# Kernel tuning notes

Measured on AMD Instinct MI355X. Metric: run time of the kernel, lower is better.

Reference implementation:

```python
import jax, jax.numpy as jnp
import numpy as np

E, M, K, I, TOPK = 8, 4096, 2048, 1408, 2
N = 2 * I  # gated: w1 produces [gate, up]


def setup_inputs() -> dict:
    key = jax.random.key(0)
    k1, k2, k3, k4, k5 = jax.random.split(key, 5)
    hidden_states = jax.random.normal(k1, (M, K), dtype=jnp.float32)
    w1 = jax.random.normal(k2, (E, N, K), dtype=jnp.float32) * 0.02
    w2 = jax.random.normal(k3, (E, K, I), dtype=jnp.float32) * 0.02
    raw = jax.random.uniform(k4, (M, TOPK), dtype=jnp.float32)
    topk_weights = raw / jnp.sum(raw, axis=-1, keepdims=True)  # router probs
    topk_ids = jax.random.randint(k5, (M, TOPK), 0, E, dtype=jnp.int32)
    return {
        "hidden_states": hidden_states,
        "w1": w1,
        "w2": w2,
        "topk_weights": topk_weights,
        "topk_ids": topk_ids,
    }


def reference(hidden_states, w1, w2, topk_weights, topk_ids):
    # MoE: permute -> grouped GEMM1 -> silu_and_mul -> grouped GEMM2 -> unpermute+reduce.
    # Dense-per-expert formulation (math-equivalent to grouped GEMM over routed tokens).
    # GEMM1: [E, M, N]
    h1 = jnp.einsum("mk,enk->emn", hidden_states, w1)
    gate, up = h1[..., :I], h1[..., I:]
    act = jax.nn.silu(gate) * up  # silu_and_mul, [E, M, I]
    # GEMM2: [E, M, K]
    y = jnp.einsum("emi,eki->emk", act, w2)
    # Unpermute: gather each token's topk expert outputs, apply router weights, reduce.
    y_tok = jnp.transpose(y, (1, 0, 2))  # [M, E, K]
    sel = jnp.take_along_axis(y_tok, topk_ids[:, :, None].astype(jnp.int32), axis=1)  # [M, topk, K]
    out = jnp.sum(sel * topk_weights[:, :, None], axis=1)  # [M, K]
    return out
```

## Files before the change

kernel.cpp:

```cpp
#include <hip/hip_runtime.h>
#include <hip/hip_bf16.h>
#include <stdint.h>

#define EXPERTS 8
#define MTOK 4096
#define KDIM 2048
#define IDIM 1408
#define NDIM 2816
#define CAP  8192

typedef __attribute__((ext_vector_type(8))) short bf16x8;
typedef __attribute__((ext_vector_type(4))) float f32x4;

__device__ __forceinline__ unsigned short f2bf(float x) {
    unsigned u = __float_as_uint(x);
    u = u + 0x7fffu + ((u >> 16) & 1u);
    return (unsigned short)(u >> 16);
}

__device__ __forceinline__ void gload16(const void* g, void* l) {
    __builtin_amdgcn_global_load_lds(
        (const __attribute__((address_space(1))) void*)g,
        (__attribute__((address_space(3))) void*)l, 16, 0, 0);
}

__global__ void __launch_bounds__(256) conv_bf16(const float* __restrict__ src,
                                                 unsigned short* __restrict__ dst, int n4) {
    int i = blockIdx.x * 256 + threadIdx.x;
    int st = gridDim.x * 256;
    for (; i < n4; i += st) {
        float4 v = reinterpret_cast<const float4*>(src)[i];
        ushort4 r;
        r.x = f2bf(v.x); r.y = f2bf(v.y); r.z = f2bf(v.z); r.w = f2bf(v.w);
        reinterpret_cast<ushort4*>(dst)[i] = r;
    }
}

__global__ void __launch_bounds__(256) router(const float* __restrict__ tw,
                                              const int* __restrict__ ids,
                                              int* __restrict__ tok, float* __restrict__ wgt,
                                              int* __restrict__ cnt) {
    int m = blockIdx.x * 256 + threadIdx.x;
    if (m >= MTOK) return;
#pragma unroll
    for (int t = 0; t < 2; t++) {
        int e = ids[m * 2 + t];
        int slot = atomicAdd(&cnt[e], 1);
        tok[e * CAP + slot] = m;
        wgt[e * CAP + slot] = tw[m * 2 + t];
    }
}

__global__ void scan_off(const int* __restrict__ cnt, int* __restrict__ off) {
    if (threadIdx.x == 0) {
        int s = 0;
        for (int e = 0; e < EXPERTS; e++) { off[e] = s; s += cnt[e]; }
    }
}

__global__ void __launch_bounds__(512, 2) gemm1_silu(
    const unsigned short* __restrict__ hsb,
    const unsigned short* __restrict__ w1b,
    const int* __restrict__ tok,
    const int* __restrict__ cnt,
    const int* __restrict__ off,
    unsigned short* __restrict__ act) {
    const int cb = blockIdx.x;
    const int rb = blockIdx.y;
    const int e  = blockIdx.z;
    const int cnt_e = cnt[e];
    if (rb * 128 >= cnt_e) return;
    const int off_e = off[e];
    const int NT = KDIM / 64;

    __shared__ __align__(16) char smem[147456];
    __shared__ int toks[128];

    const int tid = threadIdx.x;
    const int lane = tid & 63;
    const int w = tid >> 6;
    if (tid < 128) {
        int slot = rb * 128 + tid;
        toks[tid] = (slot < cnt_e) ? tok[e * CAP + slot] : 0;
    }
    __syncthreads();

    size_t sA[2]; int dA[2];
#pragma unroll
    for (int c = 0; c < 2; c++) {
        int i = c * 512 + tid;
        int row = i >> 3, gp = i & 7, gl = gp ^ (row & 7);
        sA[c] = (size_t)toks[row] * KDIM + gl * 8;
        dA[c] = i * 16;
    }
    size_t sB[4]; int dB[4];
    const size_t w1base = (size_t)e * (size_t)NDIM * KDIM;
#pragma unroll
    for (int c = 0; c < 4; c++) {
        int j = c * 512 + tid;
        int row = j >> 3, gp = j & 7, gl = gp ^ (row & 7);
        int G = row >> 4;
        int w1row = ((G & 1) ? IDIM : 0) + cb * 128 + (G >> 1) * 16 + (row & 15);
        sB[c] = w1base + (size_t)w1row * KDIM + gl * 8;
        dB[c] = 16384 + j * 16;
    }

    const int wr = w >> 2, wc = w & 3;
    const int l16 = lane & 15, lg = lane >> 4;
    int aoff[4][2], boff[4][2];
#pragma unroll
    for (int m = 0; m < 4; m++) {
        int row = wr * 64 + m * 16 + l16;
#pragma unroll
        for (int h = 0; h < 2; h++)
            aoff[m][h] = row * 128 + (((h * 4 + lg) ^ (row & 7)) * 16);
    }
#pragma unroll
    for (int n = 0; n < 4; n++) {
        int row = wc * 64 + n * 16 + l16;
#pragma unroll
        for (int h = 0; h < 2; h++)
            boff[n][h] = 16384 + row * 128 + (((h * 4 + lg) ^ (row & 7)) * 16);
    }

    f32x4 acc[4][4];
#pragma unroll
    for (int m = 0; m < 4; m++)
#pragma unroll
        for (int n = 0; n < 4; n++) acc[m][n] = {0.f, 0.f, 0.f, 0.f};

#define STG_A(t, base) { const int ko_ = (t) * 64; \
    gload16(hsb + sA[0] + ko_, (base) + dA[0]); \
    gload16(hsb + sA[1] + ko_, (base) + dA[1]); }
#define STG_B01(t, base) { const int ko_ = (t) * 64; \
    gload16(w1b + sB[0] + ko_, (base) + dB[0]); \
    gload16(w1b + sB[1] + ko_, (base) + dB[1]); }
#define STG_B23(t, base) { const int ko_ = (t) * 64; \
    gload16(w1b + sB[2] + ko_, (base) + dB[2]); \
    gload16(w1b + sB[3] + ko_, (base) + dB[3]); }

    STG_A(0, smem); STG_B01(0, smem); STG_B23(0, smem);
    { char* s1 = smem + 49152; STG_A(1, s1); STG_B01(1, s1); STG_B23(1, s1); }
    asm volatile("s_waitcnt vmcnt(6)" ::: "memory");
    __builtin_amdgcn_sched_barrier(0);
    __builtin_amdgcn_s_barrier();

    int cb_o = 0;
    int st_o = 98304;

#pragma unroll 1
    for (int t = 0; t < NT; ++t) {
        char* db = smem + cb_o;
        char* sb = smem + st_o;
        const bool stg = (t + 2 < NT);
        const int ko = (t + 2) * 64;

        bf16x8 bv0[4], bv1[4];
#pragma unroll
        for (int n = 0; n < 4; n++) {
            bv0[n] = *(const bf16x8*)(db + boff[n][0]);
            bv1[n] = *(const bf16x8*)(db + boff[n][1]);
        }
        bf16x8 a0 = *(const bf16x8*)(db + aoff[0][0]);
        bf16x8 a1 = *(const bf16x8*)(db + aoff[0][1]);
        if (stg) { gload16(hsb + sA[0] + ko, sb + dA[0]); gload16(hsb + sA[1] + ko, sb + dA[1]); }
        __builtin_amdgcn_sched_barrier(0);
        __builtin_amdgcn_s_barrier();
        asm volatile("s_waitcnt lgkmcnt(0)" ::: "memory");
        __builtin_amdgcn_sched_barrier(0);
        __builtin_amdgcn_s_setprio(1);
#pragma unroll
        for (int n = 0; n < 4; n++) acc[0][n] = __builtin_amdgcn_mfma_f32_16x16x32_bf16(a0, bv0[n], acc[0][n], 0, 0, 0);
#pragma unroll
        for (int n = 0; n < 4; n++) acc[0][n] = __builtin_amdgcn_mfma_f32_16x16x32_bf16(a1, bv1[n], acc[0][n], 0, 0, 0);
        __builtin_amdgcn_s_setprio(0);
        __builtin_amdgcn_sched_barrier(0);

        a0 = *(const bf16x8*)(db + aoff[1][0]);
        a1 = *(const bf16x8*)(db + aoff[1][1]);
        if (stg) { gload16(w1b + sB[0] + ko, sb + dB[0]); gload16(w1b + sB[1] + ko, sb + dB[1]); }
        __builtin_amdgcn_sched_barrier(0);
        __builtin_amdgcn_s_barrier();
        asm volatile("s_waitcnt lgkmcnt(0)" ::: "memory");
        __builtin_amdgcn_sched_barrier(0);
        __builtin_amdgcn_s_setprio(1);
#pragma unroll
        for (int n = 0; n < 4; n++) acc[1][n] = __builtin_amdgcn_mfma_f32_16x16x32_bf16(a0, bv0[n], acc[1][n], 0, 0, 0);
#pragma unroll
        for (int n = 0; n < 4; n++) acc[1][n] = __builtin_amdgcn_mfma_f32_16x16x32_bf16(a1, bv1[n], acc[1][n], 0, 0, 0);
        __builtin_amdgcn_s_setprio(0);
        __builtin_amdgcn_sched_barrier(0);

        a0 = *(const bf16x8*)(db + aoff[2][0]);
        a1 = *(const bf16x8*)(db + aoff[2][1]);
        if (stg) { gload16(w1b + sB[2] + ko, sb + dB[2]); gload16(w1b + sB[3] + ko, sb + dB[3]); }
        __builtin_amdgcn_sched_barrier(0);
        __builtin_amdgcn_s_barrier();
        asm volatile("s_waitcnt lgkmcnt(0)" ::: "memory");
        __builtin_amdgcn_sched_barrier(0);
        __builtin_amdgcn_s_setprio(1);
#pragma unroll
        for (int n = 0; n < 4; n++) acc[2][n] = __builtin_amdgcn_mfma_f32_16x16x32_bf16(a0, bv0[n], acc[2][n], 0, 0, 0);
#pragma unroll
        for (int n = 0; n < 4; n++) acc[2][n] = __builtin_amdgcn_mfma_f32_16x16x32_bf16(a1, bv1[n], acc[2][n], 0, 0, 0);
        __builtin_amdgcn_s_setprio(0);
        __builtin_amdgcn_sched_barrier(0);

        a0 = *(const bf16x8*)(db + aoff[3][0]);
        a1 = *(const bf16x8*)(db + aoff[3][1]);
        __builtin_amdgcn_sched_barrier(0);
        __builtin_amdgcn_s_barrier();
        asm volatile("s_waitcnt lgkmcnt(0)" ::: "memory");
        __builtin_amdgcn_sched_barrier(0);
        __builtin_amdgcn_s_setprio(1);
#pragma unroll
        for (int n = 0; n < 4; n++) acc[3][n] = __builtin_amdgcn_mfma_f32_16x16x32_bf16(a0, bv0[n], acc[3][n], 0, 0, 0);
#pragma unroll
        for (int n = 0; n < 4; n++) acc[3][n] = __builtin_amdgcn_mfma_f32_16x16x32_bf16(a1, bv1[n], acc[3][n], 0, 0, 0);
        __builtin_amdgcn_s_setprio(0);
        __builtin_amdgcn_sched_barrier(0);
        if (t + 2 < NT)      { asm volatile("s_waitcnt vmcnt(6)" ::: "memory"); }
        else if (t + 1 < NT) { asm volatile("s_waitcnt vmcnt(0)" ::: "memory"); }
        __builtin_amdgcn_sched_barrier(0);
        __builtin_amdgcn_s_barrier();

        cb_o += 49152; if (cb_o == 147456) cb_o = 0;
        st_o += 49152; if (st_o == 147456) st_o = 0;
    }
#undef STG_A
#undef STG_B01
#undef STG_B23

#pragma unroll
    for (int m = 0; m < 4; m++) {
#pragma unroll
        for (int p = 0; p < 2; p++) {
            f32x4 g4 = acc[m][p * 2];
            f32x4 u4 = acc[m][p * 2 + 1];
            int icol = cb * 128 + (wc * 2 + p) * 16 + l16;
#pragma unroll
            for (int j = 0; j < 4; j++) {
                int grow = rb * 128 + wr * 64 + m * 16 + lg * 4 + j;
                if (grow < cnt_e) {
                    float gt = g4[j], up = u4[j];
                    float s = gt / (1.f + __expf(-gt));
                    act[(size_t)(off_e + grow) * IDIM + icol] = f2bf(s * up);
                }
            }
        }
    }
}

__global__ void __launch_bounds__(256) gemm2_scatter(
    const unsigned short* __restrict__ act,
    const unsigned short* __restrict__ w2b,
    const int* __restrict__ tok,
    const float* __restrict__ wgt,
    const int* __restrict__ cnt,
    const int* __restrict__ off,
    float* __restrict__ out) {
    const int cb = blockIdx.x;
    const int rb = blockIdx.y;
    const int e  = blockIdx.z;
    const int cnt_e = cnt[e];
    if (rb * 128 >= cnt_e) return;
    const int off_e = off[e];

    __shared__ unsigned short As[128 * 32];
    __shared__ unsigned short Bs[128 * 32];
    __shared__ int toks[128];
    __shared__ float wgts[128];

    const int tid = threadIdx.x;
    const int w = tid >> 6, lane = tid & 63;
    if (tid < 128) {
        int slot = rb * 128 + tid;
        bool v = slot < cnt_e;
        toks[tid] = v ? tok[e * CAP + slot] : 0;
        wgts[tid] = v ? wgt[e * CAP + slot] : 0.f;
    }
    __syncthreads();

    const int o0 = w * 1024 + lane * 16;
    const int row0 = o0 >> 6, g0 = ((o0 >> 4) & 3) ^ ((row0 >> 1) & 3);
    const int o1 = 4096 + o0;
    const int row1 = o1 >> 6, g1 = ((o1 >> 4) & 3) ^ ((row1 >> 1) & 3);

    const int s0 = rb * 128 + row0, s1 = rb * 128 + row1;
    const size_t pa0 = (size_t)(off_e + (s0 < cnt_e ? s0 : 0)) * IDIM + g0 * 8;
    const size_t pa1 = (size_t)(off_e + (s1 < cnt_e ? s1 : 0)) * IDIM + g1 * 8;
    const size_t w2base = (size_t)e * KDIM * IDIM;
    const size_t pb0 = w2base + (size_t)(cb * 128 + row0) * IDIM + g0 * 8;
    const size_t pb1 = w2base + (size_t)(cb * 128 + row1) * IDIM + g1 * 8;

    const int wr = w >> 1, wc = w & 1;
    const int l16 = lane & 15, lg = lane >> 4;

    f32x4 acc[4][4];
#pragma unroll
    for (int m = 0; m < 4; m++)
#pragma unroll
        for (int n = 0; n < 4; n++) acc[m][n] = {0.f, 0.f, 0.f, 0.f};

    char* Ab = (char*)As;
    char* Bb = (char*)Bs;

    for (int kt = 0; kt < IDIM / 32; ++kt) {
        const int kof = kt * 32;
        gload16(act + pa0 + kof, Ab + w * 1024);
        gload16(act + pa1 + kof, Ab + 4096 + w * 1024);
        gload16(w2b + pb0 + kof, Bb + w * 1024);
        gload16(w2b + pb1 + kof, Bb + 4096 + w * 1024);
        __syncthreads();

        bf16x8 a[4], b[4];
#pragma unroll
        for (int m = 0; m < 4; m++) {
            int r = wr * 64 + m * 16 + l16;
            a[m] = *reinterpret_cast<bf16x8*>(Ab + r * 64 + ((lg ^ ((r >> 1) & 3)) * 16));
        }
#pragma unroll
        for (int n = 0; n < 4; n++) {
            int r = wc * 64 + n * 16 + l16;
            b[n] = *reinterpret_cast<bf16x8*>(Bb + r * 64 + ((lg ^ ((r >> 1) & 3)) * 16));
        }
#pragma unroll
        for (int m = 0; m < 4; m++)
#pragma unroll
            for (int n = 0; n < 4; n++)
                acc[m][n] = __builtin_amdgcn_mfma_f32_16x16x32_bf16(a[m], b[n], acc[m][n], 0, 0, 0);
        __syncthreads();
    }

#pragma unroll
    for (int m = 0; m < 4; m++) {
#pragma unroll
        for (int n = 0; n < 4; n++) {
            int kcol = cb * 128 + wc * 64 + n * 16 + l16;
#pragma unroll
            for (int j = 0; j < 4; j++) {
                int lrow = wr * 64 + m * 16 + lg * 4 + j;
                if (rb * 128 + lrow < cnt_e) {
                    atomicAdd(&out[(size_t)toks[lrow] * KDIM + kcol],
                              wgts[lrow] * acc[m][n][j]);
                }
            }
        }
    }
}

extern "C" void kernel_launch(void* const* d_in, const int* in_sizes, int n_in,
                              void* d_out, int out_size, void* d_ws, size_t ws_size,
                              hipStream_t stream) {
    const float* hs  = (const float*)d_in[0];
    const float* w1  = (const float*)d_in[1];
    const float* w2  = (const float*)d_in[2];
    const float* tw  = (const float*)d_in[3];
    const int*   ids = (const int*)d_in[4];
    float* out = (float*)d_out;

    char* ws = (char*)d_ws;
    unsigned short* w1b  = (unsigned short*)(ws);
    unsigned short* w2b  = (unsigned short*)(ws + 92274688ull);
    unsigned short* hsb  = (unsigned short*)(ws + 138412032ull);
    unsigned short* actb = (unsigned short*)(ws + 155189248ull);
    int*   tokb = (int*)  (ws + 178257920ull);
    float* wgtb = (float*)(ws + 178520064ull);
    int*   cntb = (int*)  (ws + 178782208ull);
    int*   offb = (int*)  (ws + 178782240ull);

    hipMemsetAsync(d_out, 0, (size_t)MTOK * KDIM * sizeof(float), stream);
    hipMemsetAsync(cntb, 0, 64, stream);

    conv_bf16<<<4096, 256, 0, stream>>>(w1, w1b, EXPERTS * NDIM * KDIM / 4);
    conv_bf16<<<2048, 256, 0, stream>>>(w2, w2b, EXPERTS * KDIM * IDIM / 4);
    conv_bf16<<<1024, 256, 0, stream>>>(hs, hsb, MTOK * KDIM / 4);

    router<<<MTOK / 256, 256, 0, stream>>>(tw, ids, tokb, wgtb, cntb);
    scan_off<<<1, 64, 0, stream>>>(cntb, offb);

    gemm1_silu<<<dim3(11, 64, 8), 512, 0, stream>>>(hsb, w1b, tokb, cntb, offb, actb);
    gemm2_scatter<<<dim3(16, 64, 8), 256, 0, stream>>>(actb, w2b, tokb, wgtb, cntb, offb, out);
}
```

Before: 464.3 us.

## Port gemm2 to triple-buffered 128x256 MFMA pipeline and interleave expert block order

```diff
diff --git a/kernel.cpp b/kernel.cpp
--- a/kernel.cpp
+++ b/kernel.cpp
@@ -58,6 +58,7 @@
     }
 }
 
+
 __global__ void __launch_bounds__(512, 2) gemm1_silu(
     const unsigned short* __restrict__ hsb,
     const unsigned short* __restrict__ w1b,
@@ -65,9 +66,11 @@
     const int* __restrict__ cnt,
     const int* __restrict__ off,
     unsigned short* __restrict__ act) {
-    const int cb = blockIdx.x;
-    const int rb = blockIdx.y;
-    const int e  = blockIdx.z;
+    const int bid = blockIdx.x;
+    const int e = bid & 7;
+    const int j = bid >> 3;
+    const int rb = j / 11;
+    const int cb = j - rb * 11;
     const int cnt_e = cnt[e];
     if (rb * 128 >= cnt_e) return;
     const int off_e = off[e];
@@ -97,12 +100,12 @@
     const size_t w1base = (size_t)e * (size_t)NDIM * KDIM;
 #pragma unroll
     for (int c = 0; c < 4; c++) {
-        int j = c * 512 + tid;
-        int row = j >> 3, gp = j & 7, gl = gp ^ (row & 7);
+        int jj = c * 512 + tid;
+        int row = jj >> 3, gp = jj & 7, gl = gp ^ (row & 7);
         int G = row >> 4;
         int w1row = ((G & 1) ? IDIM : 0) + cb * 128 + (G >> 1) * 16 + (row & 15);
         sB[c] = w1base + (size_t)w1row * KDIM + gl * 8;
-        dB[c] = 16384 + j * 16;
+        dB[c] = 16384 + jj * 16;
     }
 
     const int wr = w >> 2, wc = w & 3;
@@ -239,10 +242,10 @@
             f32x4 u4 = acc[m][p * 2 + 1];
             int icol = cb * 128 + (wc * 2 + p) * 16 + l16;
 #pragma unroll
-            for (int j = 0; j < 4; j++) {
-                int grow = rb * 128 + wr * 64 + m * 16 + lg * 4 + j;
+            for (int j2 = 0; j2 < 4; j2++) {
+                int grow = rb * 128 + wr * 64 + m * 16 + lg * 4 + j2;
                 if (grow < cnt_e) {
-                    float gt = g4[j], up = u4[j];
+                    float gt = g4[j2], up = u4[j2];
                     float s = gt / (1.f + __expf(-gt));
                     act[(size_t)(off_e + grow) * IDIM + icol] = f2bf(s * up);
                 }
@@ -251,7 +254,7 @@
     }
 }
 
-__global__ void __launch_bounds__(256) gemm2_scatter(
+__global__ void __launch_bounds__(512, 2) gemm2_scatter(
     const unsigned short* __restrict__ act,
     const unsigned short* __restrict__ w2b,
     const int* __restrict__ tok,
@@ -259,20 +262,23 @@
     const int* __restrict__ cnt,
     const int* __restrict__ off,
     float* __restrict__ out) {
-    const int cb = blockIdx.x;
-    const int rb = blockIdx.y;
-    const int e  = blockIdx.z;
+    const int bid = blockIdx.x;
+    const int e = bid & 7;
+    const int j = bid >> 3;
+    const int rb = j >> 3;
+    const int cb = j & 7;
     const int cnt_e = cnt[e];
     if (rb * 128 >= cnt_e) return;
     const int off_e = off[e];
-
-    __shared__ unsigned short As[128 * 32];
-    __shared__ unsigned short Bs[128 * 32];
+    const int NT = IDIM / 64;
+
+    __shared__ __align__(16) char smem[147456];
     __shared__ int toks[128];
     __shared__ float wgts[128];
 
     const int tid = threadIdx.x;
-    const int w = tid >> 6, lane = tid & 63;
+    const int lane = tid & 63;
+    const int w = tid >> 6;
     if (tid < 128) {
         int slot = rb * 128 + tid;
         bool v = slot < cnt_e;
@@ -281,20 +287,42 @@
     }
     __syncthreads();
 
-    const int o0 = w * 1024 + lane * 16;
-    const int row0 = o0 >> 6, g0 = ((o0 >> 4) & 3) ^ ((row0 >> 1) & 3);
-    const int o1 = 4096 + o0;
-    const int row1 = o1 >> 6, g1 = ((o1 >> 4) & 3) ^ ((row1 >> 1) & 3);
-
-    const int s0 = rb * 128 + row0, s1 = rb * 128 + row1;
-    const size_t pa0 = (size_t)(off_e + (s0 < cnt_e ? s0 : 0)) * IDIM + g0 * 8;
-    const size_t pa1 = (size_t)(off_e + (s1 < cnt_e ? s1 : 0)) * IDIM + g1 * 8;
-    const size_t w2base = (size_t)e * KDIM * IDIM;
-    const size_t pb0 = w2base + (size_t)(cb * 128 + row0) * IDIM + g0 * 8;
-    const size_t pb1 = w2base + (size_t)(cb * 128 + row1) * IDIM + g1 * 8;
-
-    const int wr = w >> 1, wc = w & 1;
+    size_t sA[2]; int dA[2];
+#pragma unroll
+    for (int c = 0; c < 2; c++) {
+        int i = c * 512 + tid;
+        int row = i >> 3, gp = i & 7, gl = gp ^ (row & 7);
+        int s = rb * 128 + row;
+        sA[c] = (size_t)(off_e + (s < cnt_e ? s : 0)) * IDIM + gl * 8;
+        dA[c] = i * 16;
+    }
+    size_t sB[4]; int dB[4];
+    const size_t w2base = (size_t)e * (size_t)KDIM * IDIM;
+#pragma unroll
+    for (int c = 0; c < 4; c++) {
+        int jj = c * 512 + tid;
+        int row = jj >> 3, gp = jj & 7, gl = gp ^ (row & 7);
+        sB[c] = w2base + (size_t)(cb * 256 + row) * IDIM + gl * 8;
+        dB[c] = 16384 + jj * 16;
+    }
+
+    const int wr = w >> 2, wc = w & 3;
     const int l16 = lane & 15, lg = lane >> 4;
+    int aoff[4][2], boff[4][2];
+#pragma unroll
+    for (int m = 0; m < 4; m++) {
+        int row = wr * 64 + m * 16 + l16;
+#pragma unroll
+        for (int h = 0; h < 2; h++)
+            aoff[m][h] = row * 128 + (((h * 4 + lg) ^ (row & 7)) * 16);
+    }
+#pragma unroll
+    for (int n = 0; n < 4; n++) {
+        int row = wc * 64 + n * 16 + l16;
+#pragma unroll
+        for (int h = 0; h < 2; h++)
+            boff[n][h] = 16384 + row * 128 + (((h * 4 + lg) ^ (row & 7)) * 16);
+    }
 
     f32x4 acc[4][4];
 #pragma unroll
@@ -302,47 +330,119 @@
 #pragma unroll
         for (int n = 0; n < 4; n++) acc[m][n] = {0.f, 0.f, 0.f, 0.f};
 
-    char* Ab = (char*)As;
-    char* Bb = (char*)Bs;
-
-    for (int kt = 0; kt < IDIM / 32; ++kt) {
-        const int kof = kt * 32;
-        gload16(act + pa0 + kof, Ab + w * 1024);
-        gload16(act + pa1 + kof, Ab + 4096 + w * 1024);
-        gload16(w2b + pb0 + kof, Bb + w * 1024);
-        gload16(w2b + pb1 + kof, Bb + 4096 + w * 1024);
-        __syncthreads();
-
-        bf16x8 a[4], b[4];
-#pragma unroll
-        for (int m = 0; m < 4; m++) {
-            int r = wr * 64 + m * 16 + l16;
-            a[m] = *reinterpret_cast<bf16x8*>(Ab + r * 64 + ((lg ^ ((r >> 1) & 3)) * 16));
+#define STG2_A(t, base) { const int ko_ = (t) * 64; \
+    gload16(act + sA[0] + ko_, (base) + dA[0]); \
+    gload16(act + sA[1] + ko_, (base) + dA[1]); }
+#define STG2_B01(t, base) { const int ko_ = (t) * 64; \
+    gload16(w2b + sB[0] + ko_, (base) + dB[0]); \
+    gload16(w2b + sB[1] + ko_, (base) + dB[1]); }
+#define STG2_B23(t, base) { const int ko_ = (t) * 64; \
+    gload16(w2b + sB[2] + ko_, (base) + dB[2]); \
+    gload16(w2b + sB[3] + ko_, (base) + dB[3]); }
+
+    STG2_A(0, smem); STG2_B01(0, smem); STG2_B23(0, smem);
+    { char* s1 = smem + 49152; STG2_A(1, s1); STG2_B01(1, s1); STG2_B23(1, s1); }
+    asm volatile("s_waitcnt vmcnt(6)" ::: "memory");
+    __builtin_amdgcn_sched_barrier(0);
+    __builtin_amdgcn_s_barrier();
+
+    int cb_o = 0;
+    int st_o = 98304;
+
+#pragma unroll 1
+    for (int t = 0; t < NT; ++t) {
+        char* db = smem + cb_o;
+        char* sb = smem + st_o;
+        const bool stg = (t + 2 < NT);
+        const int ko = (t + 2) * 64;
+
+        bf16x8 bv0[4], bv1[4];
+#pragma unroll
+        for (int n = 0; n < 4; n++) {
+            bv0[n] = *(const bf16x8*)(db + boff[n][0]);
+            bv1[n] = *(const bf16x8*)(db + boff[n][1]);
         }
+        bf16x8 a0 = *(const bf16x8*)(db + aoff[0][0]);
+        bf16x8 a1 = *(const bf16x8*)(db + aoff[0][1]);
+        if (stg) { gload16(act + sA[0] + ko, sb + dA[0]); gload16(act + sA[1] + ko, sb + dA[1]); }
+        __builtin_amdgcn_sched_barrier(0);
+        __builtin_amdgcn_s_barrier();
+        asm volatile("s_waitcnt lgkmcnt(0)" ::: "memory");
+        __builtin_amdgcn_sched_barrier(0);
+        __builtin_amdgcn_s_setprio(1);
+#pragma unroll
+        for (int n = 0; n < 4; n++) acc[0][n] = __builtin_amdgcn_mfma_f32_16x16x32_bf16(a0, bv0[n], acc[0][n], 0, 0, 0);
+#pragma unroll
+        for (int n = 0; n < 4; n++) acc[0][n] = __builtin_amdgcn_mfma_f32_16x16x32_bf16(a1, bv1[n], acc[0][n], 0, 0, 0);
+        __builtin_amdgcn_s_setprio(0);
+        __builtin_amdgcn_sched_barrier(0);
+
+        a0 = *(const bf16x8*)(db + aoff[1][0]);
+        a1 = *(const bf16x8*)(db + aoff[1][1]);
+        if (stg) { gload16(w2b + sB[0] + ko, sb + dB[0]); gload16(w2b + sB[1] + ko, sb + dB[1]); }
+        __builtin_amdgcn_sched_barrier(0);
+        __builtin_amdgcn_s_barrier();
+        asm volatile("s_waitcnt lgkmcnt(0)" ::: "memory");
+        __builtin_amdgcn_sched_barrier(0);
+        __builtin_amdgcn_s_setprio(1);
+#pragma unroll
+        for (int n = 0; n < 4; n++) acc[1][n] = __builtin_amdgcn_mfma_f32_16x16x32_bf16(a0, bv0[n], acc[1][n], 0, 0, 0);
+#pragma unroll
+        for (int n = 0; n < 4; n++) acc[1][n] = __builtin_amdgcn_mfma_f32_16x16x32_bf16(a1, bv1[n], acc[1][n], 0, 0, 0);
+        __builtin_amdgcn_s_setprio(0);
+        __builtin_amdgcn_sched_barrier(0);
+
+        a0 = *(const bf16x8*)(db + aoff[2][0]);
+        a1 = *(const bf16x8*)(db + aoff[2][1]);
+        if (stg) { gload16(w2b + sB[2] + ko, sb + dB[2]); gload16(w2b + sB[3] + ko, sb + dB[3]); }
+        __builtin_amdgcn_sched_barrier(0);
+        __builtin_amdgcn_s_barrier();
+        asm volatile("s_waitcnt lgkmcnt(0)" ::: "memory");
+        __builtin_amdgcn_sched_barrier(0);
+        __builtin_amdgcn_s_setprio(1);
+#pragma unroll
+        for (int n = 0; n < 4; n++) acc[2][n] = __builtin_amdgcn_mfma_f32_16x16x32_bf16(a0, bv0[n], acc[2][n], 0, 0, 0);
+#pragma unroll
+        for (int n = 0; n < 4; n++) acc[2][n] = __builtin_amdgcn_mfma_f32_16x16x32_bf16(a1, bv1[n], acc[2][n], 0, 0, 0);
+        __builtin_amdgcn_s_setprio(0);
+        __builtin_amdgcn_sched_barrier(0);
+
+        a0 = *(const bf16x8*)(db + aoff[3][0]);
+        a1 = *(const bf16x8*)(db + aoff[3][1]);
+        __builtin_amdgcn_sched_barrier(0);
+        __builtin_amdgcn_s_barrier();
+        asm volatile("s_waitcnt lgkmcnt(0)" ::: "memory");
+        __builtin_amdgcn_sched_barrier(0);
+        __builtin_amdgcn_s_setprio(1);
+#pragma unroll
+        for (int n = 0; n < 4; n++) acc[3][n] = __builtin_amdgcn_mfma_f32_16x16x32_bf16(a0, bv0[n], acc[3][n], 0, 0, 0);
+#pragma unroll
+        for (int n = 0; n < 4; n++) acc[3][n] = __builtin_amdgcn_mfma_f32_16x16x32_bf16(a1, bv1[n], acc[3][n], 0, 0, 0);
+        __builtin_amdgcn_s_setprio(0);
+        __builtin_amdgcn_sched_barrier(0);
+        if (t + 2 < NT)      { asm volatile("s_waitcnt vmcnt(6)" ::: "memory"); }
+        else if (t + 1 < NT) { asm volatile("s_waitcnt vmcnt(0)" ::: "memory"); }
+        __builtin_amdgcn_sched_barrier(0);
+        __builtin_amdgcn_s_barrier();
+
+        cb_o += 49152; if (cb_o == 147456) cb_o = 0;
+        st_o += 49152; if (st_o == 147456) st_o = 0;
+    }
+#undef STG2_A
+#undef STG2_B01
+#undef STG2_B23
+
+#pragma unroll
+    for (int m = 0; m < 4; m++) {
 #pragma unroll
         for (int n = 0; n < 4; n++) {
-            int r = wc * 64 + n * 16 + l16;
-            b[n] = *reinterpret_cast<bf16x8*>(Bb + r * 64 + ((lg ^ ((r >> 1) & 3)) * 16));
-        }
-#pragma unroll
-        for (int m = 0; m < 4; m++)
-#pragma unroll
-            for (int n = 0; n < 4; n++)
-                acc[m][n] = __builtin_amdgcn_mfma_f32_16x16x32_bf16(a[m], b[n], acc[m][n], 0, 0, 0);
-        __syncthreads();
-    }
-
-#pragma unroll
-    for (int m = 0; m < 4; m++) {
-#pragma unroll
-        for (int n = 0; n < 4; n++) {
-            int kcol = cb * 128 + wc * 64 + n * 16 + l16;
-#pragma unroll
-            for (int j = 0; j < 4; j++) {
-                int lrow = wr * 64 + m * 16 + lg * 4 + j;
+            int kcol = cb * 256 + wc * 64 + n * 16 + l16;
+#pragma unroll
+            for (int j2 = 0; j2 < 4; j2++) {
+                int lrow = wr * 64 + m * 16 + lg * 4 + j2;
                 if (rb * 128 + lrow < cnt_e) {
                     atomicAdd(&out[(size_t)toks[lrow] * KDIM + kcol],
-                              wgts[lrow] * acc[m][n][j]);
+                              wgts[lrow] * acc[m][n][j2]);
                 }
             }
         }
@@ -379,6 +479,6 @@
     router<<<MTOK / 256, 256, 0, stream>>>(tw, ids, tokb, wgtb, cntb);
     scan_off<<<1, 64, 0, stream>>>(cntb, offb);
 
-    gemm1_silu<<<dim3(11, 64, 8), 512, 0, stream>>>(hsb, w1b, tokb, cntb, offb, actb);
-    gemm2_scatter<<<dim3(16, 64, 8), 256, 0, stream>>>(actb, w2b, tokb, wgtb, cntb, offb, out);
-}
+    gemm1_silu<<<dim3(11 * 64 * 8, 1, 1), 512, 0, stream>>>(hsb, w1b, tokb, cntb, offb, actb);
+    gemm2_scatter<<<dim3(8 * 64 * 8, 1, 1), 512, 0, stream>>>(actb, w2b, tokb, wgtb, cntb, offb, out);
+}
```

Result: slower. 484.5 us (+4.4%).
